# Kernel tuning notes

Hardware: AMD Instinct MI355X
Metric: run time of the kernel (lower is better)

Reference implementation:

```python
import jax, jax.numpy as jnp
import numpy as np

N_QUBITS = 8
N_CYCLES = 4
N_LAYERS = 2  # log2(8) - 1
B = 65536

CNOT = jnp.array([[1, 0, 0, 0],
                  [0, 1, 0, 0],
                  [0, 0, 0, 1],
                  [0, 0, 1, 0]], dtype=jnp.complex64)


def apply_gate(state, U, wires):
    """Apply a (2^k x 2^k) gate U on the given wires of state (B, 2,2,...,2).
    Wire 0 is the leftmost (most significant) qubit axis."""
    k = len(wires)
    src = [w + 1 for w in wires]
    dst = list(range(1, 1 + k))
    st = jnp.moveaxis(state, src, dst)
    shp = st.shape
    st = st.reshape(shp[0], 2 ** k, -1)
    st = jnp.einsum('ij,bjr->bir', U, st)
    return jnp.moveaxis(st.reshape(shp), dst, src)


def apply_ry(state, q, angles):
    """Batched RY(angle) on qubit q; angles has shape (B,)."""
    st = jnp.moveaxis(state, q + 1, 1)  # (B, 2, rest...)
    c = jnp.cos(0.5 * angles).reshape((-1,) + (1,) * (st.ndim - 2))
    s = jnp.sin(0.5 * angles).reshape((-1,) + (1,) * (st.ndim - 2))
    s0, s1 = st[:, 0], st[:, 1]
    new = jnp.stack([c * s0 - s * s1, s * s0 + c * s1], axis=1)
    return jnp.moveaxis(new, 1, q + 1)


def crx_mat(theta):
    c = (jnp.cos(0.5 * theta) + 0j).astype(jnp.complex64)
    s = (-1j * jnp.sin(0.5 * theta)).astype(jnp.complex64)
    one = jnp.ones((), jnp.complex64)
    zero = jnp.zeros((), jnp.complex64)
    return jnp.stack([
        jnp.stack([one, zero, zero, zero]),
        jnp.stack([zero, one, zero, zero]),
        jnp.stack([zero, zero, c, s]),
        jnp.stack([zero, zero, s, c]),
    ])


def u3_mat(p):
    th, ph, lm = p[0], p[1], p[2]
    ct = (jnp.cos(0.5 * th) + 0j).astype(jnp.complex64)
    st = (jnp.sin(0.5 * th) + 0j).astype(jnp.complex64)
    el = jnp.exp(1j * lm).astype(jnp.complex64)
    ep = jnp.exp(1j * ph).astype(jnp.complex64)
    return jnp.stack([
        jnp.stack([ct, -el * st]),
        jnp.stack([ep * st, ep * el * ct]),
    ])


def expval_z(state, q):
    st = jnp.moveaxis(state, q + 1, 1)
    p = (st.real ** 2 + st.imag ** 2).reshape(st.shape[0], 2, -1).sum(-1)
    return p[:, 0] - p[:, 1]


def _forward(x, crx_theta, u3_params, w1, b1, w2, b2):
    b = x.shape[0]
    # |0...0> initial state, shape (B, 2,2,...,2)
    state = jnp.zeros((b, 2 ** N_QUBITS), jnp.complex64).at[:, 0].set(1.0)
    state = state.reshape((b,) + (2,) * N_QUBITS)
    # encoder: data re-uploading RY angle encoding + CNOT ring, n_cycles times
    for _ in range(N_CYCLES):
        for q in range(N_QUBITS):
            state = apply_ry(state, q, x[:, q])
        for q in range(N_QUBITS):
            state = apply_gate(state, CNOT, [q, (q + 1) % N_QUBITS])
    # QCNN conv/pool layers with shared weights per layer
    active = list(range(N_QUBITS))
    for layer in range(N_LAYERS):
        U = crx_mat(crx_theta[layer])
        for i in range(0, len(active) - 1, 2):
            state = apply_gate(state, U, [active[i], active[i + 1]])
        for i in range(1, len(active) - 1, 2):
            state = apply_gate(state, U, [active[i], active[i + 1]])
        remain = active[1::2]
        # mid-circuit expval in the original is discarded and does not alter state
        V = u3_mat(u3_params[layer])
        for q in remain:
            state = apply_gate(state, V, [q])
        active = remain
    feats = jnp.stack([expval_z(state, q) for q in active], axis=1)  # (B, 2)
    h = jnp.tanh(feats @ w1 + b1)
    return jax.nn.sigmoid(h @ w2 + b2)  # (B, 1)


def setup_inputs() -> dict:
    key = jax.random.key(0)
    ks = jax.random.split(key, 6)
    return {
        'x': jax.random.normal(ks[0], (B, N_QUBITS), jnp.float32),
        'crx_theta': jax.random.normal(ks[1], (N_LAYERS,), jnp.float32),
        'u3_params': jax.random.normal(ks[2], (N_LAYERS, 3), jnp.float32),
        'w1': jax.random.normal(ks[3], (2, 10), jnp.float32) * 0.5,
        'b1': jnp.zeros((10,), jnp.float32),
        'w2': jax.random.normal(ks[4], (10, 1), jnp.float32) * 0.5,
        'b2': jnp.zeros((1,), jnp.float32),
    }


def reference(x, crx_theta, u3_params, w1, b1, w2, b2):
    return _forward(x, crx_theta, u3_params, w1, b1, w2, b2)
```

## Files before the change

kernel.cpp:

```cpp
#include <hip/hip_runtime.h>


#define NQ 8
#define NE 2
#define FRAG_OFF 0
#define UR_OFF   65536
#define UI_OFF   98304

typedef _Float16 h2 __attribute__((ext_vector_type(2)));
typedef _Float16 h8 __attribute__((ext_vector_type(8)));
typedef float    f4 __attribute__((ext_vector_type(4)));

__device__ __forceinline__ float h2f(h2 v){ return __builtin_bit_cast(float, v); }
__device__ __forceinline__ h2 f2h(float v){ return __builtin_bit_cast(h2, v); }
__device__ __forceinline__ h2 u2h(unsigned u){ return __builtin_bit_cast(h2, u); }
__device__ __forceinline__ unsigned h2u(h2 v){ return __builtin_bit_cast(unsigned, v); }
__device__ __forceinline__ h2 negh(h2 v){ return u2h(h2u(v) ^ 0x80008000u); }
__device__ __forceinline__ h2 mk(float x){ return __builtin_bit_cast(h2, __builtin_amdgcn_cvt_pkrtz(x,x)); }
__device__ __forceinline__ h2 mk2(float a, float b){ return __builtin_bit_cast(h2, __builtin_amdgcn_cvt_pkrtz(a,b)); }
__device__ __forceinline__ h2 fma2h(h2 a, h2 b, h2 c){ return __builtin_elementwise_fma(a,b,c); }
__device__ __forceinline__ h2 swp(h2 v){ return __builtin_shufflevector(v,v,1,0); }

template<int CTRL>
__device__ __forceinline__ float dppf(float v){
    return __int_as_float(__builtin_amdgcn_mov_dpp(__float_as_int(v), CTRL, 0xF, 0xF, true));
}
template<int M>
__device__ __forceinline__ float sx(float v){
    if constexpr (M==1)       return dppf<0xB1>(v);
    else if constexpr (M==2)  return dppf<0x4E>(v);
    else if constexpr (M==32) return __shfl_xor(v, 32, 64);
    else return __int_as_float(__builtin_amdgcn_ds_swizzle(__float_as_int(v), (M<<10)|0x1F));
}
__device__ __forceinline__ float bperm(int ba, float v){
    return __int_as_float(__builtin_amdgcn_ds_bpermute(ba, __float_as_int(v)));
}
__device__ __forceinline__ void cmulh(h2&R, h2&I, h2 C, h2 S, h2 nS){
    h2 nR = fma2h(C, R, nS*I);
    I = fma2h(C, I, S*R);
    R = nR;
}

#define FOR_E _Pragma("unroll") for (int e = 0; e < NE; ++e)

#define RINGF() do { FOR_E { \
    h2 TA = pb ? B[e] : A[e]; \
    h2 TS = pb ? A[e] : B[e]; \
    int V0 = (int)__builtin_amdgcn_perm(h2u(TS), h2u(TA), 0x07060100u); \
    int V1 = (int)__builtin_amdgcn_perm(h2u(TA), h2u(TS), 0x07060100u); \
    unsigned r0 = (unsigned)__builtin_amdgcn_ds_bpermute(ba0, V0); \
    unsigned r1 = (unsigned)__builtin_amdgcn_ds_bpermute(ba1, V1); \
    A[e] = u2h(__builtin_amdgcn_perm(r1, r0, 0x07060100u)); \
    B[e] = u2h(__builtin_amdgcn_perm(r1, r0, 0x05040302u)); } \
} while(0)

struct P2C {
    h2 cc0,sn0,nsn0, cc1,sn1,nsn1;
    h2 uct0,ust0,nust0,usv0;
    h2 uct1,ust1,nust1;
    h2 cl1,sl1,nsl1, cp1,sp1,nsp1;
    h2 E0,E1,E2,E3,G2,G3;
    h2 Clm,Slm,nSlm,Cph,Sph,nSph;
    h2 tu1,tu3,tu5;
};

__device__ __forceinline__ P2C load_consts(const unsigned* wsu, int l){
    P2C K;
    const bool L4=(l>>4)&1, L2=(l>>2)&1, L0=l&1;
    K.cc0=u2h(wsu[0]); K.sn0=u2h(wsu[1]); K.cc1=u2h(wsu[2]); K.sn1=u2h(wsu[3]);
    K.nsn0=negh(K.sn0); K.nsn1=negh(K.sn1);
    K.uct0=u2h(wsu[4]); K.ust0=u2h(wsu[5]); K.nust0=u2h(wsu[6]); K.usv0=u2h(wsu[7]);
    K.uct1=u2h(wsu[8]); K.ust1=u2h(wsu[9]); K.nust1=u2h(wsu[10]);
    K.cl1=u2h(wsu[11]); K.sl1=u2h(wsu[12]); K.nsl1=negh(K.sl1);
    K.cp1=u2h(wsu[13]); K.sp1=u2h(wsu[14]); K.nsp1=negh(K.sp1);
    K.E0=u2h(wsu[15]); K.E1=u2h(wsu[16]); K.E2=u2h(wsu[17]);
    K.E3=u2h(wsu[18]); K.G2=u2h(wsu[19]); K.G3=u2h(wsu[20]);
    const int ki = (int)L4 + (int)L2 + (int)L0;
    K.Clm=u2h(wsu[24+ki*4+0]); K.Slm=u2h(wsu[24+ki*4+1]);
    K.Cph=u2h(wsu[24+ki*4+2]); K.Sph=u2h(wsu[24+ki*4+3]);
    K.nSlm=negh(K.Slm); K.nSph=negh(K.Sph);
    K.tu1 = L4 ? K.ust0 : K.nust0;
    K.tu3 = L2 ? K.ust0 : K.nust0;
    K.tu5 = L0 ? K.ust0 : K.nust0;
    return K;
}

#define SHF4(M) h2 oRA[NE], oIA[NE], oRB[NE], oIB[NE]; \
    FOR_E { oRA[e]=f2h(sx<M>(h2f(RA[e]))); oIA[e]=f2h(sx<M>(h2f(IA[e]))); \
            oRB[e]=f2h(sx<M>(h2f(RB[e]))); oIB[e]=f2h(sx<M>(h2f(IB[e]))); }
#define CRX_LL(CSH, M, cc, sn, nsn) do { \
    const bool ct = (l >> (CSH)) & 1; \
    SHF4(M) \
    if (ct) { FOR_E { \
        RA[e] = fma2h(cc, RA[e], (sn)*oIA[e]); IA[e] = fma2h(cc, IA[e], (nsn)*oRA[e]); \
        RB[e] = fma2h(cc, RB[e], (sn)*oIB[e]); IB[e] = fma2h(cc, IB[e], (nsn)*oRB[e]); } } \
} while(0)
#define RYC0(M, T) do { \
    SHF4(M) \
    FOR_E { \
    RA[e] = fma2h(K.uct0, RA[e], (T)*oRA[e]); IA[e] = fma2h(K.uct0, IA[e], (T)*oIA[e]); \
    RB[e] = fma2h(K.uct0, RB[e], (T)*oRB[e]); IB[e] = fma2h(K.uct0, IB[e], (T)*oIB[e]); } \
} while(0)

__device__ __forceinline__ void phase2run(const int l, const P2C& K,
    const h2* A, const h2* B, h2* RA, h2* RB, h2* IA, h2* IB)
{
    const bool L5=(l>>5)&1, L2=(l>>2)&1, L0=l&1;
    FOR_E { RA[e]=A[e]; RB[e]=B[e]; IA[e]=(h2){0,0}; IB[e]=(h2){0,0}; }

    {   h2 oA[NE], oB[NE];
        FOR_E { oA[e]=f2h(sx<16>(h2f(RA[e]))); oB[e]=f2h(sx<16>(h2f(RB[e]))); }
        if (L5){ FOR_E {
            IA[e] = K.nsn0*oA[e]; RA[e] = K.cc0*RA[e];
            IB[e] = K.nsn0*oB[e]; RB[e] = K.cc0*RB[e]; } }
    }
    CRX_LL(3, 4, K.cc0, K.sn0, K.nsn0);
    CRX_LL(1, 1, K.cc0, K.sn0, K.nsn0);
    FOR_E {
        h2 oI = swp(IB[e]), oR = swp(RB[e]);
        RB[e] = fma2h(K.cc0, RB[e], K.sn0*oI);
        IB[e] = fma2h(K.cc0, IB[e], K.nsn0*oR);
    }
    CRX_LL(4, 8, K.cc0, K.sn0, K.nsn0);
    CRX_LL(2, 2, K.cc0, K.sn0, K.nsn0);
    if (L0) { FOR_E {
        h2 nRA = fma2h(K.cc0, RA[e], K.sn0*IB[e]);
        h2 nRB = fma2h(K.cc0, RB[e], K.sn0*IA[e]);
        h2 nIA = fma2h(K.cc0, IA[e], K.nsn0*RB[e]);
        h2 nIB = fma2h(K.cc0, IB[e], K.nsn0*RA[e]);
        RA[e]=nRA; RB[e]=nRB; IA[e]=nIA; IB[e]=nIB; } }
    FOR_E { cmulh(RA[e],IA[e],K.Clm,K.Slm,K.nSlm); cmulh(RB[e],IB[e],K.Clm,K.Slm,K.nSlm); }
    RYC0(16, K.tu1);
    RYC0(4,  K.tu3);
    RYC0(1,  K.tu5);
    FOR_E {
        h2 sA=swp(RA[e]), sB=swp(RB[e]), tA=swp(IA[e]), tB=swp(IB[e]);
        RA[e] = fma2h(K.uct0, RA[e], K.usv0*sA); RB[e] = fma2h(K.uct0, RB[e], K.usv0*sB);
        IA[e] = fma2h(K.uct0, IA[e], K.usv0*tA); IB[e] = fma2h(K.uct0, IB[e], K.usv0*tB);
    }
    FOR_E { cmulh(RA[e],IA[e],K.Cph,K.Sph,K.nSph); cmulh(RB[e],IB[e],K.Cph,K.Sph,K.nSph); }

    CRX_LL(4, 4, K.cc1, K.sn1, K.nsn1);
    if (L0) { FOR_E {
        h2 sIA=swp(IA[e]), sRA=swp(RA[e]), sIB=swp(IB[e]), sRB=swp(RB[e]);
        RA[e] = fma2h(K.cc1, RA[e], K.sn1*sIA); IA[e] = fma2h(K.cc1, IA[e], K.nsn1*sRA);
        RB[e] = fma2h(K.cc1, RB[e], K.sn1*sIB); IB[e] = fma2h(K.cc1, IB[e], K.nsn1*sRB); } }
    CRX_LL(2, 1, K.cc1, K.sn1, K.nsn1);
    {
        if (L2){ FOR_E { cmulh(RA[e],IA[e],K.cl1,K.sl1,K.nsl1); cmulh(RB[e],IB[e],K.cl1,K.sl1,K.nsl1); } }
        h2 T = L2 ? K.ust1 : K.nust1;
        SHF4(4)
        FOR_E {
            RA[e] = fma2h(K.uct1, RA[e], T*oRA[e]); IA[e] = fma2h(K.uct1, IA[e], T*oIA[e]);
            RB[e] = fma2h(K.uct1, RB[e], T*oRB[e]); IB[e] = fma2h(K.uct1, IB[e], T*oIB[e]);
        }
        if (L2){ FOR_E { cmulh(RA[e],IA[e],K.cp1,K.sp1,K.nsp1); cmulh(RB[e],IB[e],K.cp1,K.sp1,K.nsp1); } }
    }
    FOR_E {
        h2 sR=swp(RA[e]), sI=swp(IA[e]);
        h2 nR = fma2h(K.E3,sI, fma2h(K.E2,IA[e], fma2h(K.E1,sR, K.E0*RA[e])));
        h2 nI = fma2h(K.G3,sR, fma2h(K.G2,RA[e], fma2h(K.E1,sI, K.E0*IA[e])));
        RA[e]=nR; IA[e]=nI;
        h2 sR2=swp(RB[e]), sI2=swp(IB[e]);
        h2 nR2 = fma2h(K.E3,sI2, fma2h(K.E2,IB[e], fma2h(K.E1,sR2, K.E0*RB[e])));
        h2 nI2 = fma2h(K.G3,sR2, fma2h(K.G2,RB[e], fma2h(K.E1,sI2, K.E0*IB[e])));
        RB[e]=nR2; IB[e]=nI2;
    }
}

__global__ __launch_bounds__(1024) void qcnn_prep_u(
    const float* __restrict__ crx, const float* __restrict__ u3p,
    unsigned* __restrict__ ws)
{
    __shared__ unsigned cws[48];
    if (threadIdx.x == 0){
        auto PK=[](float lo, float hi)->unsigned{
            unsigned a=__builtin_bit_cast(unsigned short,(_Float16)lo);
            unsigned b=__builtin_bit_cast(unsigned short,(_Float16)hi);
            return a | (b<<16);
        };
        float sc0,cc0,sc1,cc1;
        __sincosf(0.5f*crx[0],&sc0,&cc0);
        __sincosf(0.5f*crx[1],&sc1,&cc1);
        cws[0]=PK(cc0,cc0); cws[1]=PK(sc0,sc0); cws[2]=PK(cc1,cc1); cws[3]=PK(sc1,sc1);
        float th0=u3p[0], ph0=u3p[1], lm0=u3p[2];
        float ust0,uct0; __sincosf(0.5f*th0,&ust0,&uct0);
        cws[4]=PK(uct0,uct0); cws[5]=PK(ust0,ust0); cws[6]=PK(-ust0,-ust0); cws[7]=PK(-ust0,ust0);
        float th1=u3p[3], ph1=u3p[4], lm1=u3p[5];
        float ust1,uct1; __sincosf(0.5f*th1,&ust1,&uct1);
        float sl1,cl1;   __sincosf(lm1,&sl1,&cl1);
        float sp1,cp1;   __sincosf(ph1,&sp1,&cp1);
        cws[8]=PK(uct1,uct1); cws[9]=PK(ust1,ust1); cws[10]=PK(-ust1,-ust1);
        cws[11]=PK(cl1,cl1); cws[12]=PK(sl1,sl1); cws[13]=PK(cp1,cp1); cws[14]=PK(sp1,sp1);
        float cpl1=cp1*cl1-sp1*sl1, spl1=sp1*cl1+cp1*sl1;
        float u01r=-ust1*cl1, u01i=-ust1*sl1;
        float u10r= ust1*cp1, u10i= ust1*sp1;
        float u11r= uct1*cpl1, u11i= uct1*spl1;
        cws[15]=PK(uct1,u11r); cws[16]=PK(u01r,u10r); cws[17]=PK(0.f,-u11i);
        cws[18]=PK(-u01i,-u10i); cws[19]=PK(0.f,u11i); cws[20]=PK(u01i,u10i);
        for(int k=0;k<4;++k){
            float kf=(float)k, sA,cA,sB,cB,sA2,cA2,sB2,cB2;
            __sincosf(lm0*kf,      &sA,&cA);
            __sincosf(lm0*(kf+1.f),&sB,&cB);
            __sincosf(ph0*kf,      &sA2,&cA2);
            __sincosf(ph0*(kf+1.f),&sB2,&cB2);
            unsigned* q = cws + 24 + k*4;
            q[0]=PK(cA,cB); q[1]=PK(sA,sB); q[2]=PK(cA2,cB2); q[3]=PK(sA2,sB2);
        }
    }
    __syncthreads();

    const int l = threadIdx.x & 63;
    const int w = threadIdx.x >> 6;
    const P2C K = load_consts(cws, l);
    const bool pb = __builtin_popcount(l) & 1;
    const int ba0 = (((l&32)|((l^(l>>1))&31)) << 2);
    const int ba1 = ba0 ^ (48<<2);

    for (int it = 0; it < 8; ++it){
        const int j0 = w*16 + it*2;
        h2 A[NE], B[NE];
        FOR_E {
            A[e]=(h2){0,0}; B[e]=(h2){0,0};
            const int j = j0 + e;
            if (l == (j >> 2)){
                const int slot = j & 3;
                const _Float16 one = (_Float16)1.f;
                if      (slot==0) A[e].x = one;
                else if (slot==1) A[e].y = one;
                else if (slot==2) B[e].x = one;
                else              B[e].y = one;
            }
        }
        RINGF();
        h2 RA[NE], RB[NE], IA[NE], IB[NE];
        phase2run(l, K, A, B, RA, RB, IA, IB);
        FOR_E {
            const int j = j0 + e;
            *(uint2*)(ws + UR_OFF + j*128 + l*2) = make_uint2(h2u(RA[e]), h2u(RB[e]));
            *(uint2*)(ws + UI_OFF + j*128 + l*2) = make_uint2(h2u(IA[e]), h2u(IB[e]));
        }
    }
}

__global__ void qcnn_prep_frag(unsigned* __restrict__ ws){
    const int T = blockIdx.x*256 + threadIdx.x;
    const int chunk = T >> 6, l = T & 63;
    const int ct = chunk >> 4, ri = (chunk >> 3) & 1, ks = chunk & 7;
    const unsigned short* U = (const unsigned short*)(ws + (ri ? UI_OFF : UR_OFF));
    const int n = ct*16 + (l & 15);
    const int g = l >> 4;
    unsigned d[4];
#pragma unroll
    for (int p = 0; p < 4; ++p){
        const int k0 = ks*32 + g*8 + 2*p;
        unsigned lo = U[k0*256 + n];
        unsigned hi = U[(k0+1)*256 + n];
        d[p] = lo | (hi << 16);
    }
    uint4 v; v.x=d[0]; v.y=d[1]; v.z=d[2]; v.w=d[3];
    *(uint4*)(ws + FRAG_OFF + chunk*256 + l*4) = v;
}

__global__ __launch_bounds__(1024) void qcnn_kernel(
    const float* __restrict__ x,
    const unsigned* __restrict__ wsu,
    const float* __restrict__ w1,
    const float* __restrict__ b1,
    const float* __restrict__ w2,
    const float* __restrict__ b2,
    float* __restrict__ out,
    int Btot)
{
    __shared__ __align__(16) unsigned char Sl[32*512];
    __shared__ float parts[16][2][32];
    const int tid = threadIdx.x;
    const int l = tid & 63;
    const int w = tid >> 6;
    const int eblk = blockIdx.x * 32;
    const int e0 = eblk + w*NE;
    const bool L5=(l>>5)&1, L4=(l>>4)&1, L3=(l>>3)&1, L2=(l>>2)&1, L1=(l>>1)&1, L0=l&1;

    const bool pb = __builtin_popcount(l) & 1;
    const int ba0 = (((l&32)|((l^(l>>1))&31)) << 2);
    const int ba1 = ba0 ^ (48<<2);

    const bool bits[6]={L5,L4,L3,L2,L1,L0};
    unsigned sm[6];
#pragma unroll
    for(int q=0;q<6;++q) sm[q] = bits[q] ? 0u : 0x80008000u;

    h2 cH[NE][6], tsH[NE][6];
    h2 c6h[NE], s6h[NE], ns6h[NE], c7h[NE], sv7h[NE];
    h2 A[NE], B[NE];
    FOR_E {
        const int ee = (e0 + e < Btot) ? (e0 + e) : (Btot - 1);
        const float4* xv = (const float4*)(x + ee*NQ);
        float4 xa=xv[0], xb=xv[1];
        float ang[8]={xa.x,xa.y,xa.z,xa.w,xb.x,xb.y,xb.z,xb.w};
        float cq[8], sq[8];
#pragma unroll
        for(int q=0;q<8;++q) __sincosf(0.5f*ang[q], &sq[q], &cq[q]);
#pragma unroll
        for(int q=0;q<6;++q){
            cH[e][q]=mk(cq[q]);
            tsH[e][q]=u2h(h2u(mk(sq[q])) ^ sm[q]);
        }
        c6h[e]=mk(cq[6]); s6h[e]=mk(sq[6]); ns6h[e]=negh(s6h[e]);
        c7h[e]=mk(cq[7]); sv7h[e]=mk2(-sq[7], sq[7]);
        float pl = (L5?sq[0]:cq[0])*(L4?sq[1]:cq[1])*(L3?sq[2]:cq[2])
                 * (L2?sq[3]:cq[3])*(L1?sq[4]:cq[4])*(L0?sq[5]:cq[5]);
        float pc6=pl*cq[6], ps6=pl*sq[6];
        A[e] = mk2(pc6*cq[7], pc6*sq[7]);
        B[e] = mk2(ps6*cq[7], ps6*sq[7]);
    }

#define RY_L(q, M) do { FOR_E { \
    h2 oA = f2h(sx<M>(h2f(A[e]))), oB = f2h(sx<M>(h2f(B[e]))); \
    A[e] = fma2h(cH[e][q], A[e], tsH[e][q]*oA); \
    B[e] = fma2h(cH[e][q], B[e], tsH[e][q]*oB); } \
} while(0)

    RINGF();
#pragma unroll
    for(int cyc=0;cyc<3;++cyc){
        RY_L(0,32); RY_L(1,16); RY_L(2,8); RY_L(3,4); RY_L(4,2); RY_L(5,1);
        FOR_E { h2 nA = fma2h(c6h[e], A[e], ns6h[e]*B[e]);
                h2 nB = fma2h(s6h[e], A[e], c6h[e]*B[e]);
                A[e]=nA; B[e]=nB; }
        FOR_E { A[e] = fma2h(c7h[e], A[e], sv7h[e]*swp(A[e]));
                B[e] = fma2h(c7h[e], B[e], sv7h[e]*swp(B[e])); }
        if (cyc < 2) RINGF();
    }

    FOR_E {
        const int r = w*NE + e;
        const unsigned off = ((unsigned)(r*512 + l*8)) ^ (((unsigned)(r&7))<<4);
        *(uint2*)(Sl + off) = make_uint2(h2u(A[e]), h2u(B[e]));
    }
    __syncthreads();

    f4 aR0={0,0,0,0}, aI0={0,0,0,0}, aR1={0,0,0,0}, aI1={0,0,0,0};
    const int m0 = l & 15, g = l >> 4;
    const unsigned swzA = ((unsigned)(m0 & 7)) << 4;
    const unsigned* frag = wsu + FRAG_OFF;
#pragma unroll
    for (int ks = 0; ks < 8; ++ks){
        const unsigned c = (unsigned)(ks*64 + g*16);
        h8 a0 = *(const h8*)(Sl + (((unsigned)(m0*512)        + c) ^ swzA));
        h8 a1 = *(const h8*)(Sl + (((unsigned)((m0+16)*512)   + c) ^ swzA));
        h8 br = *(const h8*)(frag + (w*16 +     ks)*256 + l*4);
        h8 bi = *(const h8*)(frag + (w*16 + 8 + ks)*256 + l*4);
        aR0 = __builtin_amdgcn_mfma_f32_16x16x32_f16(a0, br, aR0, 0, 0, 0);
        aR1 = __builtin_amdgcn_mfma_f32_16x16x32_f16(a1, br, aR1, 0, 0, 0);
        aI0 = __builtin_amdgcn_mfma_f32_16x16x32_f16(a0, bi, aI0, 0, 0, 0);
        aI1 = __builtin_amdgcn_mfma_f32_16x16x32_f16(a1, bi, aI1, 0, 0, 0);
    }

    const float s3 = (w & 1) ? -1.f : 1.f;
    const float s7 = (l & 1) ? -1.f : 1.f;
    float f0a[4], f1a[4], f0b[4], f1b[4];
#pragma unroll
    for (int r = 0; r < 4; ++r){
        float nv0 = fmaf(aR0[r], aR0[r], aI0[r]*aI0[r]);
        float nv1 = fmaf(aR1[r], aR1[r], aI1[r]*aI1[r]);
        f0a[r] = s3*nv0; f1a[r] = s7*nv0;
        f0b[r] = s3*nv1; f1b[r] = s7*nv1;
    }
#pragma unroll
    for (int r = 0; r < 4; ++r){
        f0a[r] += sx<1>(f0a[r]); f0a[r] += sx<2>(f0a[r]); f0a[r] += sx<4>(f0a[r]); f0a[r] += sx<8>(f0a[r]);
        f1a[r] += sx<1>(f1a[r]); f1a[r] += sx<2>(f1a[r]); f1a[r] += sx<4>(f1a[r]); f1a[r] += sx<8>(f1a[r]);
        f0b[r] += sx<1>(f0b[r]); f0b[r] += sx<2>(f0b[r]); f0b[r] += sx<4>(f0b[r]); f0b[r] += sx<8>(f0b[r]);
        f1b[r] += sx<1>(f1b[r]); f1b[r] += sx<2>(f1b[r]); f1b[r] += sx<4>(f1b[r]); f1b[r] += sx<8>(f1b[r]);
    }
    if ((l & 15) == 0){
        const int rb = g*4;
#pragma unroll
        for (int r = 0; r < 4; ++r){
            parts[w][0][rb+r]    = f0a[r];
            parts[w][1][rb+r]    = f1a[r];
            parts[w][0][16+rb+r] = f0b[r];
            parts[w][1][16+rb+r] = f1b[r];
        }
    }
    __syncthreads();

    if (tid < 512){
        const int elem = tid >> 4, k = tid & 15;
        float F0 = 0.f, F1 = 0.f;
#pragma unroll
        for (int ww = 0; ww < 16; ++ww){
            F0 += parts[ww][0][elem];
            F1 += parts[ww][1][elem];
        }
        float contrib = 0.0f;
        if (k < 10){
            float z = fmaf(F0, w1[k], fmaf(F1, w1[10+k], b1[k]));
            float ex = __expf(2.0f*z);
            contrib = ((ex-1.0f)/(ex+1.0f)) * w2[k];
        }
        contrib += sx<1>(contrib);
        contrib += sx<2>(contrib);
        contrib += sx<4>(contrib);
        contrib += sx<8>(contrib);
        if (k == 0 && eblk + elem < Btot){
            out[eblk + elem] = 1.0f/(1.0f + __expf(-(contrib + b2[0])));
        }
    }
}

extern "C" void kernel_launch(void* const* d_in, const int* in_sizes, int n_in,
                              void* d_out, int out_size, void* d_ws, size_t ws_size,
                              hipStream_t stream) {
    const float* x   = (const float*)d_in[0];
    const float* crx = (const float*)d_in[1];
    const float* u3p = (const float*)d_in[2];
    const float* w1  = (const float*)d_in[3];
    const float* b1  = (const float*)d_in[4];
    const float* w2  = (const float*)d_in[5];
    const float* b2  = (const float*)d_in[6];
    float* out = (float*)d_out;
    unsigned* ws = (unsigned*)d_ws;

    const int B = in_sizes[0] / NQ;
    hipLaunchKernelGGL(qcnn_prep_u,    dim3(1),  dim3(1024), 0, stream, crx, u3p, ws);
    hipLaunchKernelGGL(qcnn_prep_frag, dim3(64), dim3(256),  0, stream, ws);
    const int grid = (B + 31) / 32;
    hipLaunchKernelGGL(qcnn_kernel, dim3(grid), dim3(1024), 0, stream,
                       x, ws, w1, b1, w2, b2, out, B);
}
```

Before: 138.5 us.

## Split angle trig into separate kernel, parallelize U prep, relayout LDS tiles

Moves the per-element sincos of input angles into a new pre-kernel that writes cos/sin to workspace, which the main kernel then reads. The single-block unitary prep is spread over 8 blocks instead of looping 8 times in one block. The LDS A-tile layout is changed to a k-slice-major swizzle, and the cross-wave partial-sum array is transposed so the final reduction uses float4 loads. The trade is an extra launch and twice the input bytes read through global memory, against a much shorter serial prep stage and cheaper shared-memory access.

```diff
diff --git a/kernel.cpp b/kernel.cpp
--- a/kernel.cpp
+++ b/kernel.cpp
@@ -6,6 +6,7 @@
 #define FRAG_OFF 0
 #define UR_OFF   65536
 #define UI_OFF   98304
+#define ANG_OFF  131072
 
 typedef _Float16 h2 __attribute__((ext_vector_type(2)));
 typedef _Float16 h8 __attribute__((ext_vector_type(8)));
@@ -31,9 +32,6 @@
     else if constexpr (M==2)  return dppf<0x4E>(v);
     else if constexpr (M==32) return __shfl_xor(v, 32, 64);
     else return __int_as_float(__builtin_amdgcn_ds_swizzle(__float_as_int(v), (M<<10)|0x1F));
-}
-__device__ __forceinline__ float bperm(int ba, float v){
-    return __int_as_float(__builtin_amdgcn_ds_bpermute(ba, __float_as_int(v)));
 }
 __device__ __forceinline__ void cmulh(h2&R, h2&I, h2 C, h2 S, h2 nS){
     h2 nR = fma2h(C, R, nS*I);
@@ -166,6 +164,24 @@
         h2 nI2 = fma2h(K.G3,sR2, fma2h(K.G2,RB[e], fma2h(K.E1,sI2, K.E0*IB[e])));
         RB[e]=nR2; IB[e]=nI2;
     }
+}
+
+__global__ __launch_bounds__(256) void qcnn_angles(
+    const float* __restrict__ x, float* __restrict__ ang, int Btot)
+{
+    const int e = blockIdx.x*256 + threadIdx.x;
+    if (e >= Btot) return;
+    const float4* xv = (const float4*)(x + e*NQ);
+    float4 xa=xv[0], xb=xv[1];
+    float a[8]={xa.x,xa.y,xa.z,xa.w,xb.x,xb.y,xb.z,xb.w};
+    float c[8], s[8];
+#pragma unroll
+    for(int q=0;q<8;++q) __sincosf(0.5f*a[q], &s[q], &c[q]);
+    float4* ov = (float4*)(ang + e*16);
+    ov[0] = make_float4(c[0],c[1],c[2],c[3]);
+    ov[1] = make_float4(c[4],c[5],c[6],c[7]);
+    ov[2] = make_float4(s[0],s[1],s[2],s[3]);
+    ov[3] = make_float4(s[4],s[5],s[6],s[7]);
 }
 
 __global__ __launch_bounds__(1024) void qcnn_prep_u(
@@ -217,29 +233,27 @@
     const int ba0 = (((l&32)|((l^(l>>1))&31)) << 2);
     const int ba1 = ba0 ^ (48<<2);
 
-    for (int it = 0; it < 8; ++it){
-        const int j0 = w*16 + it*2;
-        h2 A[NE], B[NE];
-        FOR_E {
-            A[e]=(h2){0,0}; B[e]=(h2){0,0};
-            const int j = j0 + e;
-            if (l == (j >> 2)){
-                const int slot = j & 3;
-                const _Float16 one = (_Float16)1.f;
-                if      (slot==0) A[e].x = one;
-                else if (slot==1) A[e].y = one;
-                else if (slot==2) B[e].x = one;
-                else              B[e].y = one;
-            }
-        }
-        RINGF();
-        h2 RA[NE], RB[NE], IA[NE], IB[NE];
-        phase2run(l, K, A, B, RA, RB, IA, IB);
-        FOR_E {
-            const int j = j0 + e;
-            *(uint2*)(ws + UR_OFF + j*128 + l*2) = make_uint2(h2u(RA[e]), h2u(RB[e]));
-            *(uint2*)(ws + UI_OFF + j*128 + l*2) = make_uint2(h2u(IA[e]), h2u(IB[e]));
-        }
+    const int j0 = blockIdx.x*32 + w*2;
+    h2 A[NE], B[NE];
+    FOR_E {
+        A[e]=(h2){0,0}; B[e]=(h2){0,0};
+        const int j = j0 + e;
+        if (l == (j >> 2)){
+            const int slot = j & 3;
+            const _Float16 one = (_Float16)1.f;
+            if      (slot==0) A[e].x = one;
+            else if (slot==1) A[e].y = one;
+            else if (slot==2) B[e].x = one;
+            else              B[e].y = one;
+        }
+    }
+    RINGF();
+    h2 RA[NE], RB[NE], IA[NE], IB[NE];
+    phase2run(l, K, A, B, RA, RB, IA, IB);
+    FOR_E {
+        const int j = j0 + e;
+        *(uint2*)(ws + UR_OFF + j*128 + l*2) = make_uint2(h2u(RA[e]), h2u(RB[e]));
+        *(uint2*)(ws + UI_OFF + j*128 + l*2) = make_uint2(h2u(IA[e]), h2u(IB[e]));
     }
 }
 
@@ -263,7 +277,6 @@
 }
 
 __global__ __launch_bounds__(1024) void qcnn_kernel(
-    const float* __restrict__ x,
     const unsigned* __restrict__ wsu,
     const float* __restrict__ w1,
     const float* __restrict__ b1,
@@ -272,8 +285,8 @@
     float* __restrict__ out,
     int Btot)
 {
-    __shared__ __align__(16) unsigned char Sl[32*512];
-    __shared__ float parts[16][2][32];
+    __shared__ __align__(16) unsigned char Sl[16*1024];
+    __shared__ __align__(16) float parts[2][32][16];
     const int tid = threadIdx.x;
     const int l = tid & 63;
     const int w = tid >> 6;
@@ -293,14 +306,13 @@
     h2 cH[NE][6], tsH[NE][6];
     h2 c6h[NE], s6h[NE], ns6h[NE], c7h[NE], sv7h[NE];
     h2 A[NE], B[NE];
+    const float* angv = (const float*)(wsu + ANG_OFF);
     FOR_E {
         const int ee = (e0 + e < Btot) ? (e0 + e) : (Btot - 1);
-        const float4* xv = (const float4*)(x + ee*NQ);
-        float4 xa=xv[0], xb=xv[1];
-        float ang[8]={xa.x,xa.y,xa.z,xa.w,xb.x,xb.y,xb.z,xb.w};
-        float cq[8], sq[8];
-#pragma unroll
-        for(int q=0;q<8;++q) __sincosf(0.5f*ang[q], &sq[q], &cq[q]);
+        const float4* av = (const float4*)(angv + ee*16);
+        float4 ca=av[0], cb=av[1], sa=av[2], sb=av[3];
+        float cq[8]={ca.x,ca.y,ca.z,ca.w,cb.x,cb.y,cb.z,cb.w};
+        float sq[8]={sa.x,sa.y,sa.z,sa.w,sb.x,sb.y,sb.z,sb.w};
 #pragma unroll
         for(int q=0;q<6;++q){
             cH[e][q]=mk(cq[q]);
@@ -335,20 +347,20 @@
 
     FOR_E {
         const int r = w*NE + e;
-        const unsigned off = ((unsigned)(r*512 + l*8)) ^ (((unsigned)(r&7))<<4);
+        const int mblk = r >> 4, rr = r & 15;
+        const int ks = l >> 3, g = (l >> 1) & 3, p = l & 1;
+        const unsigned off = (unsigned)(((mblk*8 + ks) << 10)
+                             + (((rr + 16*g) ^ ks) << 4) + (p << 3));
         *(uint2*)(Sl + off) = make_uint2(h2u(A[e]), h2u(B[e]));
     }
     __syncthreads();
 
     f4 aR0={0,0,0,0}, aI0={0,0,0,0}, aR1={0,0,0,0}, aI1={0,0,0,0};
-    const int m0 = l & 15, g = l >> 4;
-    const unsigned swzA = ((unsigned)(m0 & 7)) << 4;
     const unsigned* frag = wsu + FRAG_OFF;
 #pragma unroll
     for (int ks = 0; ks < 8; ++ks){
-        const unsigned c = (unsigned)(ks*64 + g*16);
-        h8 a0 = *(const h8*)(Sl + (((unsigned)(m0*512)        + c) ^ swzA));
-        h8 a1 = *(const h8*)(Sl + (((unsigned)((m0+16)*512)   + c) ^ swzA));
+        h8 a0 = *(const h8*)(Sl + ((     ks) << 10) + ((l ^ ks) << 4));
+        h8 a1 = *(const h8*)(Sl + ((8 +  ks) << 10) + ((l ^ ks) << 4));
         h8 br = *(const h8*)(frag + (w*16 +     ks)*256 + l*4);
         h8 bi = *(const h8*)(frag + (w*16 + 8 + ks)*256 + l*4);
         aR0 = __builtin_amdgcn_mfma_f32_16x16x32_f16(a0, br, aR0, 0, 0, 0);
@@ -359,6 +371,7 @@
 
     const float s3 = (w & 1) ? -1.f : 1.f;
     const float s7 = (l & 1) ? -1.f : 1.f;
+    const int g = l >> 4;
     float f0a[4], f1a[4], f0b[4], f1b[4];
 #pragma unroll
     for (int r = 0; r < 4; ++r){
@@ -378,22 +391,24 @@
         const int rb = g*4;
 #pragma unroll
         for (int r = 0; r < 4; ++r){
-            parts[w][0][rb+r]    = f0a[r];
-            parts[w][1][rb+r]    = f1a[r];
-            parts[w][0][16+rb+r] = f0b[r];
-            parts[w][1][16+rb+r] = f1b[r];
+            parts[0][rb+r]   [w] = f0a[r];
+            parts[1][rb+r]   [w] = f1a[r];
+            parts[0][16+rb+r][w] = f0b[r];
+            parts[1][16+rb+r][w] = f1b[r];
         }
     }
     __syncthreads();
 
     if (tid < 512){
         const int elem = tid >> 4, k = tid & 15;
-        float F0 = 0.f, F1 = 0.f;
-#pragma unroll
-        for (int ww = 0; ww < 16; ++ww){
-            F0 += parts[ww][0][elem];
-            F1 += parts[ww][1][elem];
-        }
+        const float4* p0 = (const float4*)&parts[0][elem][0];
+        const float4* p1 = (const float4*)&parts[1][elem][0];
+        float4 u0=p0[0], u1=p0[1], u2=p0[2], u3=p0[3];
+        float4 v0=p1[0], v1=p1[1], v2=p1[2], v3=p1[3];
+        float F0 = ((u0.x+u0.y)+(u0.z+u0.w)) + ((u1.x+u1.y)+(u1.z+u1.w))
+                 + ((u2.x+u2.y)+(u2.z+u2.w)) + ((u3.x+u3.y)+(u3.z+u3.w));
+        float F1 = ((v0.x+v0.y)+(v0.z+v0.w)) + ((v1.x+v1.y)+(v1.z+v1.w))
+                 + ((v2.x+v2.y)+(v2.z+v2.w)) + ((v3.x+v3.y)+(v3.z+v3.w));
         float contrib = 0.0f;
         if (k < 10){
             float z = fmaf(F0, w1[k], fmaf(F1, w1[10+k], b1[k]));
@@ -424,9 +439,11 @@
     unsigned* ws = (unsigned*)d_ws;
 
     const int B = in_sizes[0] / NQ;
-    hipLaunchKernelGGL(qcnn_prep_u,    dim3(1),  dim3(1024), 0, stream, crx, u3p, ws);
+    hipLaunchKernelGGL(qcnn_angles, dim3((B+255)/256), dim3(256), 0, stream,
+                       x, (float*)(ws + ANG_OFF), B);
+    hipLaunchKernelGGL(qcnn_prep_u,    dim3(8),  dim3(1024), 0, stream, crx, u3p, ws);
     hipLaunchKernelGGL(qcnn_prep_frag, dim3(64), dim3(256),  0, stream, ws);
     const int grid = (B + 31) / 32;
     hipLaunchKernelGGL(qcnn_kernel, dim3(grid), dim3(1024), 0, stream,
-                       x, ws, w1, b1, w2, b2, out, B);
-}
+                       ws, w1, b1, w2, b2, out, B);
+}
```

After: 121.9 us. 12.0% less time.
